# Kernel optimization log

Hardware: AMD Instinct MI355X
Metric: run time of the kernel (lower is better)

The kernel has to match this reference:

```python
import jax, jax.numpy as jnp
import numpy as np

# Geometry: 256x256 image, 16x16 superpixel grid (cell=16), K=256, C=20 features, B=4.
B, H, W, C, KG = 4, 256, 256, 20, 16
K = KG * KG
CELL = H // KG
BIG_DIST = 1e4  # additive distance for non-neighbor superpixels


def setup_inputs() -> dict:
    key = jax.random.key(0)
    kf, = jax.random.split(key, 1)
    # initial hard pixel->superpixel grid assignment (get_spixel_init)
    gy = jnp.arange(H) // CELL
    gx = jnp.arange(W) // CELL
    spixel_init = (gy[:, None] * KG + gx[None, :]).reshape(-1).astype(jnp.int32)  # [N]
    # 9-neighborhood validity mask (compute_neighbor_spix_idx)
    ky = jnp.arange(K) // KG
    kx = jnp.arange(K) % KG
    pgy = spixel_init // KG
    pgx = spixel_init % KG
    valid = ((jnp.abs(pgy[:, None] - ky[None, :]) <= 1)
             & (jnp.abs(pgx[:, None] - kx[None, :]) <= 1)).astype(jnp.float32)  # [N, K]
    adjust = (1.0 - valid) * BIG_DIST  # [N, K]
    features = jax.random.normal(kf, (B, H * W, C), dtype=jnp.float32)  # CNN output, flattened
    return {
        "features": features,
        "valid_spixel": valid,
        "adjust_dist": adjust,
        "spixel_init": spixel_init,
        "iter_EM": 10,
    }


def _e_step(mean, features, valid_spixel, adjust_dist):
    # squared distances via ||f||^2 - 2 f.m + ||m||^2 (bmm form)
    feat_sq = jnp.sum(features * features, axis=-1)        # [B, N]
    mean_sq = jnp.sum(mean * mean, axis=-1)                # [B, K]
    dot = jnp.einsum('bnc,bkc->bnk', features, mean)       # [B, N, K]
    dist_sq = feat_sq[:, :, None] - 2.0 * dot + mean_sq[:, None, :]
    dist_sq = dist_sq * valid_spixel[None] + adjust_dist[None]
    # std = 1/sqrt(2) => 2*std^2 = 1, so softmax argument is -dist_sq
    return jax.nn.softmax(-dist_sq, axis=2)                # [B, N, K]


def _m_step(features, posteriors):
    # L1-normalize posteriors over the pixel axis (dim=1), then weighted mean
    col = jnp.maximum(jnp.sum(posteriors, axis=1, keepdims=True), 1e-12)
    post_norm = posteriors / col
    return jnp.einsum('bnk,bnc->bkc', post_norm, features)  # [B, K, C]


def reference(features, valid_spixel, adjust_dist, spixel_init, iter_EM):
    # compute_init_spixel_feat: mean of features within each initial superpixel (detached in torch)
    n = features.shape[1]
    sums = jax.vmap(lambda f: jax.ops.segment_sum(f, spixel_init, num_segments=K))(features)  # [B, K, C]
    counts = jax.ops.segment_sum(jnp.ones((n,), features.dtype), spixel_init, num_segments=K)  # [K]
    mean = jax.lax.stop_gradient(sums / jnp.maximum(counts, 1.0)[None, :, None])
    for _ in range(int(iter_EM) - 1):
        posteriors = _e_step(mean, features, valid_spixel, adjust_dist)
        mean = _m_step(features, posteriors)
    return _e_step(mean, features, valid_spixel, adjust_dist)
```

## Files before the change

kernel.cpp:

```cpp
#include <hip/hip_runtime.h>
#include <hip/hip_cooperative_groups.h>


#define NBATCH 4
#define WIMG   256
#define NC     20
#define NCS    21
#define SCELL  32
#define NKG    16
#define NK     256
#define NPIX   65536
#define CELLSZ 16
#define LDST   260

__device__ __forceinline__ float dot4f(const float4 a, const float4 b) {
    return fmaf(a.x, b.x, fmaf(a.y, b.y, fmaf(a.z, b.z, a.w * b.w)));
}

__device__ __forceinline__ void load_feat(const float* __restrict__ feat, int b, int n, float f[NC]) {
    const float4* fp = (const float4*)(feat + ((size_t)b * NPIX + n) * NC);
    #pragma unroll
    for (int i = 0; i < 5; ++i) {
        float4 v = fp[i];
        f[4 * i + 0] = v.x; f[4 * i + 1] = v.y; f[4 * i + 2] = v.z; f[4 * i + 3] = v.w;
    }
}


__device__ __forceinline__ void gate(int* done, int target, int b, int cy, int cx, int t) {
    if (t < 25) {
        int dy = t / 5 - 2, dx = t % 5 - 2;
        int ky = cy + dy, kx = cx + dx;
        if (ky >= 0 && ky < NKG && kx >= 0 && kx < NKG) {
            int idx = b * NK + ky * NKG + kx;
            while (__hip_atomic_load(&done[idx], __ATOMIC_RELAXED, __HIP_MEMORY_SCOPE_AGENT) < target) {
                __builtin_amdgcn_s_sleep(1);
            }
        }
    }
    __syncthreads();
}

__device__ __forceinline__ void e_step_p(const float* f, int b, int cy, int cx,
                                         const float* __restrict__ Sprev,
                                         const float* rrL, const float* mtL, float p[9]) {
    float a[9];
    float amax = -1e30f;
    #pragma unroll
    for (int dy = -1; dy <= 1; ++dy) {
        #pragma unroll
        for (int dx = -1; dx <= 1; ++dx) {
            int j = (dy + 1) * 3 + (dx + 1);
            int ky = cy + dy, kx = cx + dx;
            if (ky >= 0 && ky < NKG && kx >= 0 && kx < NKG) {
                const float* sp = Sprev + ((size_t)(b * NK + ky * NKG + kx)) * SCELL;
                float dots = 0.f;
                #pragma unroll
                for (int c = 0; c < NC; ++c) dots = fmaf(f[c], sp[c], dots);
                a[j] = 2.0f * rrL[j] * dots - mtL[j];
                amax = fmaxf(amax, a[j]);
            } else {
                a[j] = -1e30f;
            }
        }
    }
    float esum = 0.f;
    #pragma unroll
    for (int j = 0; j < 9; ++j) {
        float e = (a[j] > -1e29f) ? __expf(a[j] - amax) : 0.0f;
        p[j] = e;
        esum += e;
    }
    float inv = 1.0f / esum;
    #pragma unroll
    for (int j = 0; j < 9; ++j) p[j] *= inv;
}

__global__ __launch_bounds__(256, 4) void k_ssn_df(const float* __restrict__ feat,
                                                   int* __restrict__ done,
                                                   float* __restrict__ Sbase,
                                                   float* __restrict__ out) {
    __shared__ float fT[NCS * LDST];
    __shared__ float pT[9 * LDST];
    __shared__ float part[21 * 8 * 9];
    __shared__ float rrL[9], mtL[9];

    const size_t SBUF = (size_t)NBATCH * NK * SCELL;
    int blk = blockIdx.x;
    int b = blk >> 8, k0 = blk & 255;
    int cy = k0 >> 4, cx = k0 & 15;
    int t = threadIdx.x;
    int ly = t >> 4, lx = t & 15;
    int n = (cy * CELLSZ + ly) * WIMG + cx * CELLSZ + lx;

    float f[NC];
    load_feat(feat, b, n, f);
    #pragma unroll
    for (int c = 0; c < NC; ++c) fT[c * LDST + t] = f[c];
    fT[NC * LDST + t] = 1.0f;
    __syncthreads();

    if (t < NCS) {
        float s;
        if (t == NC) {
            s = 256.0f;
        } else {
            s = 0.f;
            const float4* row = (const float4*)&fT[t * LDST];
            #pragma unroll 4
            for (int i = 0; i < 64; ++i) { float4 v = row[i]; s += v.x + v.y + v.z + v.w; }
        }
        __hip_atomic_store(&Sbase[((size_t)(b * NK + k0)) * SCELL + t], s,
                           __ATOMIC_RELAXED, __HIP_MEMORY_SCOPE_AGENT);
    }
    __syncthreads();
    if (t == 0) __hip_atomic_fetch_add(&done[blk], 1, __ATOMIC_RELAXED, __HIP_MEMORY_SCOPE_AGENT);

    for (int it = 1; it <= 9; ++it) {
        const float* __restrict__ Sprev = Sbase + (size_t)(it - 1) * SBUF;
        float* Snext = Sbase + (size_t)it * SBUF;

        gate(done, it, b, cy, cx, t);

        if (t < 9) {
            int dy = t / 3 - 1, dx = t % 3 - 1;
            int ky = cy + dy, kx = cx + dx;
            if (ky >= 0 && ky < NKG && kx >= 0 && kx < NKG) {
                const float* sp = Sprev + ((size_t)(b * NK + ky * NKG + kx)) * SCELL;
                float ssq = 0.f;
                #pragma unroll
                for (int c = 0; c < NC; ++c) ssq = fmaf(sp[c], sp[c], ssq);
                float r = 1.0f / fmaxf(sp[NC], 1e-12f);
                rrL[t] = r;
                mtL[t] = ssq * r * r;
            }
        }
        __syncthreads();

        float p[9];
        e_step_p(f, b, cy, cx, Sprev, rrL, mtL, p);
        #pragma unroll
        for (int j = 0; j < 9; ++j) pT[j * LDST + t] = p[j];
        __syncthreads();

        if (t < 168) {
            int tile = t >> 3, kid = t & 7;
            int j0 = (tile / 7) * 3, c0 = (tile % 7) * 3;
            float acc[3][3] = {};
            #pragma unroll
            for (int ch = 0; ch < 8; ++ch) {
                int nb = kid * 32 + (((ch + kid) & 7) << 2);
                float4 pv[3], fv[3];
                #pragma unroll
                for (int jj = 0; jj < 3; ++jj) pv[jj] = *(const float4*)&pT[(j0 + jj) * LDST + nb];
                #pragma unroll
                for (int cc = 0; cc < 3; ++cc) fv[cc] = *(const float4*)&fT[(c0 + cc) * LDST + nb];
                #pragma unroll
                for (int jj = 0; jj < 3; ++jj)
                    #pragma unroll
                    for (int cc = 0; cc < 3; ++cc)
                        acc[jj][cc] += dot4f(pv[jj], fv[cc]);
            }
            #pragma unroll
            for (int jj = 0; jj < 3; ++jj)
                #pragma unroll
                for (int cc = 0; cc < 3; ++cc)
                    part[tile * 72 + kid * 9 + jj * 3 + cc] = acc[jj][cc];
        }
        __syncthreads();
        if (t < 189) {
            int j = t / 21, c = t % 21;
            int tile = (j / 3) * 7 + (c / 3);
            int elem = (j % 3) * 3 + (c % 3);
            float s = 0.f;
            #pragma unroll
            for (int kid = 0; kid < 8; ++kid) s += part[tile * 72 + kid * 9 + elem];
            int ky = cy + (j / 3) - 1, kx = cx + (j % 3) - 1;
            if (ky >= 0 && ky < NKG && kx >= 0 && kx < NKG)
                atomicAdd(&Snext[((size_t)(b * NK + ky * NKG + kx)) * SCELL + c], s);
        }
        __syncthreads();
        if (t == 0) __hip_atomic_fetch_add(&done[blk], 1, __ATOMIC_RELAXED, __HIP_MEMORY_SCOPE_AGENT);
    }

    {
        const float* __restrict__ Sprev = Sbase + (size_t)9 * SBUF;
        gate(done, 10, b, cy, cx, t);
        if (t < 9) {
            int dy = t / 3 - 1, dx = t % 3 - 1;
            int ky = cy + dy, kx = cx + dx;
            if (ky >= 0 && ky < NKG && kx >= 0 && kx < NKG) {
                const float* sp = Sprev + ((size_t)(b * NK + ky * NKG + kx)) * SCELL;
                float ssq = 0.f;
                #pragma unroll
                for (int c = 0; c < NC; ++c) ssq = fmaf(sp[c], sp[c], ssq);
                float r = 1.0f / fmaxf(sp[NC], 1e-12f);
                rrL[t] = r;
                mtL[t] = ssq * r * r;
            }
        }
        __syncthreads();

        float p[9];
        e_step_p(f, b, cy, cx, Sprev, rrL, mtL, p);
        #pragma unroll
        for (int j = 0; j < 9; ++j) pT[j * LDST + t] = p[j];
        __syncthreads();

        int wv = t >> 6, ln = t & 63;
        int j4[4];
        #pragma unroll
        for (int q = 0; q < 4; ++q) {
            int k = 4 * ln + q;
            int ky = k >> 4, kx = k & 15;
            int dy = ky - cy, dx = kx - cx;
            j4[q] = (dy >= -1 && dy <= 1 && dx >= -1 && dx <= 1) ? (dy + 1) * 3 + (dx + 1) : -1;
        }
        for (int i = 0; i < 64; ++i) {
            int pix = wv * 64 + i;
            int py = pix >> 4, px = pix & 15;
            int np = (cy * CELLSZ + py) * WIMG + cx * CELLSZ + px;
            float4 o;
            o.x = (j4[0] >= 0) ? pT[j4[0] * LDST + pix] : 0.0f;
            o.y = (j4[1] >= 0) ? pT[j4[1] * LDST + pix] : 0.0f;
            o.z = (j4[2] >= 0) ? pT[j4[2] * LDST + pix] : 0.0f;
            o.w = (j4[3] >= 0) ? pT[j4[3] * LDST + pix] : 0.0f;
            size_t rowoff = ((size_t)(b * NPIX + np)) * (size_t)NK;
            *(float4*)(out + rowoff + 4 * ln) = o;
        }
    }
}

__device__ __forceinline__ void e_step_fb(const float* f, int b, int cy, int cx,
                                          const float* __restrict__ Sprev, float p[9]) {
    float a[9];
    float amax = -1e30f;
    #pragma unroll
    for (int dy = -1; dy <= 1; ++dy) {
        #pragma unroll
        for (int dx = -1; dx <= 1; ++dx) {
            int j = (dy + 1) * 3 + (dx + 1);
            int ky = cy + dy, kx = cx + dx;
            if (ky >= 0 && ky < NKG && kx >= 0 && kx < NKG) {
                const float* sp = Sprev + ((size_t)(b * NK + ky * NKG + kx)) * NCS;
                float dots = 0.f, ssq = 0.f;
                #pragma unroll
                for (int c = 0; c < NC; ++c) {
                    float sv = sp[c];
                    dots = fmaf(f[c], sv, dots);
                    ssq  = fmaf(sv, sv, ssq);
                }
                float col = fmaxf(sp[NC], 1e-12f);
                float r = 1.0f / col;
                a[j] = 2.0f * r * dots - (r * r) * ssq;
                amax = fmaxf(amax, a[j]);
            } else {
                a[j] = -1e30f;
            }
        }
    }
    float esum = 0.f;
    #pragma unroll
    for (int j = 0; j < 9; ++j) {
        float e = (a[j] > -1e29f) ? __expf(a[j] - amax) : 0.0f;
        p[j] = e;
        esum += e;
    }
    float inv = 1.0f / esum;
    #pragma unroll
    for (int j = 0; j < 9; ++j) p[j] *= inv;
}

__global__ __launch_bounds__(256, 4) void k_init(const float* __restrict__ feat,
                                                 float* __restrict__ S0,
                                                 float* __restrict__ S1) {
    __shared__ float fT[NC * LDST];
    int blk = blockIdx.x;
    int b = blk >> 8, k0 = blk & 255;
    int cy = k0 >> 4, cx = k0 & 15;
    int t = threadIdx.x;
    int ly = t >> 4, lx = t & 15;
    int n = (cy * CELLSZ + ly) * WIMG + cx * CELLSZ + lx;
    float f[NC];
    load_feat(feat, b, n, f);
    #pragma unroll
    for (int c = 0; c < NC; ++c) fT[c * LDST + t] = f[c];
    __syncthreads();
    if (t < NCS) {
        float s;
        if (t == NC) {
            s = 256.0f;
        } else {
            s = 0.f;
            const float4* row = (const float4*)&fT[t * LDST];
            #pragma unroll 4
            for (int i = 0; i < 64; ++i) { float4 v = row[i]; s += v.x + v.y + v.z + v.w; }
        }
        size_t off = ((size_t)(b * NK + k0)) * NCS + t;
        S0[off] = s;
        S1[off] = 0.0f;
    }
}

__global__ __launch_bounds__(256, 4) void k_em(const float* __restrict__ feat,
                                               const float* __restrict__ Sprev,
                                               float* __restrict__ Snext,
                                               float* __restrict__ Szero) {
    __shared__ float fT[NCS * LDST];
    __shared__ float pT[9 * LDST];
    __shared__ float part[21 * 8 * 9];
    int blk = blockIdx.x;
    int b = blk >> 8, k0 = blk & 255;
    int cy = k0 >> 4, cx = k0 & 15;
    int t = threadIdx.x;
    int ly = t >> 4, lx = t & 15;
    int n = (cy * CELLSZ + ly) * WIMG + cx * CELLSZ + lx;
    float f[NC];
    load_feat(feat, b, n, f);
    #pragma unroll
    for (int c = 0; c < NC; ++c) fT[c * LDST + t] = f[c];
    fT[NC * LDST + t] = 1.0f;
    float p[9];
    e_step_fb(f, b, cy, cx, Sprev, p);
    #pragma unroll
    for (int j = 0; j < 9; ++j) pT[j * LDST + t] = p[j];
    __syncthreads();
    if (t < 168) {
        int tile = t >> 3, kid = t & 7;
        int j0 = (tile / 7) * 3, c0 = (tile % 7) * 3;
        float acc[3][3] = {};
        #pragma unroll
        for (int ch = 0; ch < 8; ++ch) {
            int nb = kid * 32 + (((ch + kid) & 7) << 2);
            float4 pv[3], fv[3];
            #pragma unroll
            for (int jj = 0; jj < 3; ++jj) pv[jj] = *(const float4*)&pT[(j0 + jj) * LDST + nb];
            #pragma unroll
            for (int cc = 0; cc < 3; ++cc) fv[cc] = *(const float4*)&fT[(c0 + cc) * LDST + nb];
            #pragma unroll
            for (int jj = 0; jj < 3; ++jj)
                #pragma unroll
                for (int cc = 0; cc < 3; ++cc)
                    acc[jj][cc] += dot4f(pv[jj], fv[cc]);
        }
        #pragma unroll
        for (int jj = 0; jj < 3; ++jj)
            #pragma unroll
            for (int cc = 0; cc < 3; ++cc)
                part[tile * 72 + kid * 9 + jj * 3 + cc] = acc[jj][cc];
    }
    __syncthreads();
    if (t < 189) {
        int j = t / 21, c = t % 21;
        int tile = (j / 3) * 7 + (c / 3);
        int elem = (j % 3) * 3 + (c % 3);
        float s = 0.f;
        #pragma unroll
        for (int kid = 0; kid < 8; ++kid) s += part[tile * 72 + kid * 9 + elem];
        int ky = cy + (j / 3) - 1, kx = cx + (j % 3) - 1;
        if (ky >= 0 && ky < NKG && kx >= 0 && kx < NKG)
            atomicAdd(&Snext[((size_t)(b * NK + ky * NKG + kx)) * NCS + c], s);
    }
    if (t < NCS) Szero[((size_t)(b * NK + k0)) * NCS + t] = 0.0f;
}

__global__ __launch_bounds__(256, 4) void k_final(const float* __restrict__ feat,
                                                  const float* __restrict__ Sprev,
                                                  float* __restrict__ out) {
    __shared__ float pT[9 * LDST];
    int blk = blockIdx.x;
    int b = blk >> 8, k0 = blk & 255;
    int cy = k0 >> 4, cx = k0 & 15;
    int t = threadIdx.x;
    int ly = t >> 4, lx = t & 15;
    int n = (cy * CELLSZ + ly) * WIMG + cx * CELLSZ + lx;
    float f[NC];
    load_feat(feat, b, n, f);
    float p[9];
    e_step_fb(f, b, cy, cx, Sprev, p);
    #pragma unroll
    for (int j = 0; j < 9; ++j) pT[j * LDST + t] = p[j];
    __syncthreads();
    int wv = t >> 6, ln = t & 63;
    int j4[4];
    #pragma unroll
    for (int q = 0; q < 4; ++q) {
        int k = 4 * ln + q;
        int ky = k >> 4, kx = k & 15;
        int dy = ky - cy, dx = kx - cx;
        j4[q] = (dy >= -1 && dy <= 1 && dx >= -1 && dx <= 1) ? (dy + 1) * 3 + (dx + 1) : -1;
    }
    for (int i = 0; i < 64; ++i) {
        int pix = wv * 64 + i;
        int py = pix >> 4, px = pix & 15;
        int np = (cy * CELLSZ + py) * WIMG + cx * CELLSZ + px;
        float4 o;
        o.x = (j4[0] >= 0) ? pT[j4[0] * LDST + pix] : 0.0f;
        o.y = (j4[1] >= 0) ? pT[j4[1] * LDST + pix] : 0.0f;
        o.z = (j4[2] >= 0) ? pT[j4[2] * LDST + pix] : 0.0f;
        o.w = (j4[3] >= 0) ? pT[j4[3] * LDST + pix] : 0.0f;
        size_t rowoff = ((size_t)(b * NPIX + np)) * (size_t)NK;
        *(float4*)(out + rowoff + 4 * ln) = o;
    }
}

extern "C" void kernel_launch(void* const* d_in, const int* in_sizes, int n_in,
                              void* d_out, int out_size, void* d_ws, size_t ws_size,
                              hipStream_t stream) {
    (void)in_sizes; (void)n_in; (void)out_size;
    const float* feat = (const float*)d_in[0];
    float* out = (float*)d_out;

    int* done = (int*)d_ws;
    float* Sbase = (float*)((char*)d_ws + 4096);
    const size_t zbytes = 4096 + 10 * (size_t)NBATCH * NK * SCELL * sizeof(float);

    dim3 grid(NBATCH * NK), block(256);
    if (ws_size >= zbytes) {
        hipMemsetAsync(d_ws, 0, zbytes, stream);
        void* args[] = { (void*)&feat, (void*)&done, (void*)&Sbase, (void*)&out };
        hipError_t err = hipLaunchCooperativeKernel((const void*)k_ssn_df, grid, block, args, 0, stream);
        if (err == hipSuccess) return;
    }

    const size_t SB = (size_t)NBATCH * NK * NCS;
    float* s0 = (float*)d_ws;
    float* s1 = (float*)d_ws + SB;
    float* s2 = (float*)d_ws + 2 * SB;
    float* bufs[3] = { s0, s1, s2 };
    k_init<<<grid, block, 0, stream>>>(feat, bufs[0], bufs[1]);
    for (int i = 1; i <= 9; ++i)
        k_em<<<grid, block, 0, stream>>>(feat, bufs[(i - 1) % 3], bufs[i % 3], bufs[(i + 1) % 3]);
    k_final<<<grid, block, 0, stream>>>(feat, bufs[0], out);
}
```

Before: 673.7 us.

## Replace atomicAdd scatter with per-block partial stores and neighbor gather reduction

Each block now writes its 9x21 partial M-step sums to a private slot instead of doing float atomicAdds into neighbors' accumulators. A second neighbor-only gate lets each block gather its own superpixel sum from the 9 neighbors' partials. This removes atomic contention and the large workspace memset, since only the done counters are zeroed now. Other changes: the 3x3 superpixel stats are staged in shared memory, blocks are remapped to group rows per XCD, and the output uses nontemporal stores. The cost is twice as many gate waits per iteration.

```diff
diff --git a/kernel.cpp b/kernel.cpp
--- a/kernel.cpp
+++ b/kernel.cpp
@@ -6,15 +6,24 @@
 #define WIMG   256
 #define NC     20
 #define NCS    21
-#define SCELL  32
+#define PSTR   24
 #define NKG    16
 #define NK     256
 #define NPIX   65536
 #define CELLSZ 16
 #define LDST   260
 
+typedef float floatx4 __attribute__((ext_vector_type(4)));
+
 __device__ __forceinline__ float dot4f(const float4 a, const float4 b) {
     return fmaf(a.x, b.x, fmaf(a.y, b.y, fmaf(a.z, b.z, a.w * b.w)));
+}
+
+__device__ __forceinline__ float ld_sc1(const float* p) {
+    return __hip_atomic_load(p, __ATOMIC_RELAXED, __HIP_MEMORY_SCOPE_AGENT);
+}
+__device__ __forceinline__ void st_sc1(float* p, float v) {
+    __hip_atomic_store(p, v, __ATOMIC_RELAXED, __HIP_MEMORY_SCOPE_AGENT);
 }
 
 __device__ __forceinline__ void load_feat(const float* __restrict__ feat, int b, int n, float f[NC]) {
@@ -26,24 +35,22 @@
     }
 }
 
-
-__device__ __forceinline__ void gate(int* done, int target, int b, int cy, int cx, int t) {
-    if (t < 25) {
-        int dy = t / 5 - 2, dx = t % 5 - 2;
-        int ky = cy + dy, kx = cx + dx;
+__device__ __forceinline__ void gate9(int* done, int target, int b, int cy, int cx, int t) {
+    if (t < 9) {
+        int ky = cy + t / 3 - 1, kx = cx + t % 3 - 1;
         if (ky >= 0 && ky < NKG && kx >= 0 && kx < NKG) {
             int idx = b * NK + ky * NKG + kx;
             while (__hip_atomic_load(&done[idx], __ATOMIC_RELAXED, __HIP_MEMORY_SCOPE_AGENT) < target) {
-                __builtin_amdgcn_s_sleep(1);
+                __builtin_amdgcn_s_sleep(2);
             }
         }
     }
     __syncthreads();
 }
 
-__device__ __forceinline__ void e_step_p(const float* f, int b, int cy, int cx,
-                                         const float* __restrict__ Sprev,
-                                         const float* rrL, const float* mtL, float p[9]) {
+__device__ __forceinline__ void e_step_l(const float* f, int cy, int cx,
+                                         const float* sS, const float* rrL, const float* mtL,
+                                         float p[9]) {
     float a[9];
     float amax = -1e30f;
     #pragma unroll
@@ -53,7 +60,7 @@
             int j = (dy + 1) * 3 + (dx + 1);
             int ky = cy + dy, kx = cx + dx;
             if (ky >= 0 && ky < NKG && kx >= 0 && kx < NKG) {
-                const float* sp = Sprev + ((size_t)(b * NK + ky * NKG + kx)) * SCELL;
+                const float* sp = sS + j * PSTR;
                 float dots = 0.f;
                 #pragma unroll
                 for (int c = 0; c < NC; ++c) dots = fmaf(f[c], sp[c], dots);
@@ -76,19 +83,22 @@
     for (int j = 0; j < 9; ++j) p[j] *= inv;
 }
 
-__global__ __launch_bounds__(256, 4) void k_ssn_df(const float* __restrict__ feat,
-                                                   int* __restrict__ done,
-                                                   float* __restrict__ Sbase,
-                                                   float* __restrict__ out) {
+__global__ __launch_bounds__(256, 4) void k_ssn_g(const float* __restrict__ feat,
+                                                  int* __restrict__ done,
+                                                  float* __restrict__ Sc,
+                                                  float* __restrict__ Pp,
+                                                  float* __restrict__ out) {
     __shared__ float fT[NCS * LDST];
     __shared__ float pT[9 * LDST];
     __shared__ float part[21 * 8 * 9];
+    __shared__ float sS[9 * PSTR];
     __shared__ float rrL[9], mtL[9];
 
-    const size_t SBUF = (size_t)NBATCH * NK * SCELL;
     int blk = blockIdx.x;
-    int b = blk >> 8, k0 = blk & 255;
-    int cy = k0 >> 4, cx = k0 & 15;
+    int xcd = blk & 7, q = blk >> 3;
+    int b = q >> 5, r = q & 31;
+    int cy = (xcd << 1) | (r >> 4), cx = r & 15;
+    int k0 = cy * NKG + cx;
     int t = threadIdx.x;
     int ly = t >> 4, lx = t & 15;
     int n = (cy * CELLSZ + ly) * WIMG + cx * CELLSZ + lx;
@@ -110,35 +120,41 @@
             #pragma unroll 4
             for (int i = 0; i < 64; ++i) { float4 v = row[i]; s += v.x + v.y + v.z + v.w; }
         }
-        __hip_atomic_store(&Sbase[((size_t)(b * NK + k0)) * SCELL + t], s,
-                           __ATOMIC_RELAXED, __HIP_MEMORY_SCOPE_AGENT);
-    }
-    __syncthreads();
-    if (t == 0) __hip_atomic_fetch_add(&done[blk], 1, __ATOMIC_RELAXED, __HIP_MEMORY_SCOPE_AGENT);
+        st_sc1(&Sc[((size_t)(b * NK + k0)) * PSTR + t], s);
+    }
+    __syncthreads();
+    if (t == 0) __hip_atomic_fetch_add(&done[b * NK + k0], 1, __ATOMIC_RELAXED, __HIP_MEMORY_SCOPE_AGENT);
 
     for (int it = 1; it <= 9; ++it) {
-        const float* __restrict__ Sprev = Sbase + (size_t)(it - 1) * SBUF;
-        float* Snext = Sbase + (size_t)it * SBUF;
-
-        gate(done, it, b, cy, cx, t);
-
+        const float* Sp = Sc + ((size_t)(it - 1) * NBATCH + b) * NK * PSTR;
+        float* Pit = Pp + ((size_t)it * NBATCH + b) * NK * 9 * PSTR;
+        float* Snx = Sc + ((size_t)it * NBATCH + b) * NK * PSTR;
+
+        gate9(done, 2 * it - 1, b, cy, cx, t);
+
+        if (t < 189) {
+            int j = t / 21, c = t % 21;
+            int ky = cy + j / 3 - 1, kx = cx + j % 3 - 1;
+            if (ky >= 0 && ky < NKG && kx >= 0 && kx < NKG)
+                sS[j * PSTR + c] = ld_sc1(&Sp[(size_t)(ky * NKG + kx) * PSTR + c]);
+        }
+        __syncthreads();
         if (t < 9) {
-            int dy = t / 3 - 1, dx = t % 3 - 1;
-            int ky = cy + dy, kx = cx + dx;
+            int ky = cy + t / 3 - 1, kx = cx + t % 3 - 1;
             if (ky >= 0 && ky < NKG && kx >= 0 && kx < NKG) {
-                const float* sp = Sprev + ((size_t)(b * NK + ky * NKG + kx)) * SCELL;
+                const float* sp = &sS[t * PSTR];
                 float ssq = 0.f;
                 #pragma unroll
                 for (int c = 0; c < NC; ++c) ssq = fmaf(sp[c], sp[c], ssq);
-                float r = 1.0f / fmaxf(sp[NC], 1e-12f);
-                rrL[t] = r;
-                mtL[t] = ssq * r * r;
-            }
+                float rr = 1.0f / fmaxf(sp[NC], 1e-12f);
+                rrL[t] = rr;
+                mtL[t] = ssq * rr * rr;
+            } else { rrL[t] = 1.0f; mtL[t] = 0.0f; }
         }
         __syncthreads();
 
         float p[9];
-        e_step_p(f, b, cy, cx, Sprev, rrL, mtL, p);
+        e_step_l(f, cy, cx, sS, rrL, mtL, p);
         #pragma unroll
         for (int j = 0; j < 9; ++j) pT[j * LDST + t] = p[j];
         __syncthreads();
@@ -175,34 +191,60 @@
             float s = 0.f;
             #pragma unroll
             for (int kid = 0; kid < 8; ++kid) s += part[tile * 72 + kid * 9 + elem];
-            int ky = cy + (j / 3) - 1, kx = cx + (j % 3) - 1;
+            int ky = cy + j / 3 - 1, kx = cx + j % 3 - 1;
             if (ky >= 0 && ky < NKG && kx >= 0 && kx < NKG)
-                atomicAdd(&Snext[((size_t)(b * NK + ky * NKG + kx)) * SCELL + c], s);
-        }
-        __syncthreads();
-        if (t == 0) __hip_atomic_fetch_add(&done[blk], 1, __ATOMIC_RELAXED, __HIP_MEMORY_SCOPE_AGENT);
+                st_sc1(&Pit[((size_t)k0 * 9 + j) * PSTR + c], s);
+        }
+        __syncthreads();
+        if (t == 0) __hip_atomic_fetch_add(&done[b * NK + k0], 1, __ATOMIC_RELAXED, __HIP_MEMORY_SCOPE_AGENT);
+
+        gate9(done, 2 * it, b, cy, cx, t);
+
+        if (t < NCS) {
+            float s = 0.f;
+            #pragma unroll
+            for (int u = -1; u <= 1; ++u) {
+                #pragma unroll
+                for (int v = -1; v <= 1; ++v) {
+                    int py = cy + u, px = cx + v;
+                    if (py >= 0 && py < NKG && px >= 0 && px < NKG) {
+                        int e = (1 - u) * 3 + (1 - v);
+                        s += ld_sc1(&Pit[((size_t)(py * NKG + px) * 9 + e) * PSTR + t]);
+                    }
+                }
+            }
+            st_sc1(&Snx[(size_t)k0 * PSTR + t], s);
+        }
+        __syncthreads();
+        if (t == 0) __hip_atomic_fetch_add(&done[b * NK + k0], 1, __ATOMIC_RELAXED, __HIP_MEMORY_SCOPE_AGENT);
     }
 
     {
-        const float* __restrict__ Sprev = Sbase + (size_t)9 * SBUF;
-        gate(done, 10, b, cy, cx, t);
+        const float* Sp = Sc + ((size_t)9 * NBATCH + b) * NK * PSTR;
+        gate9(done, 19, b, cy, cx, t);
+        if (t < 189) {
+            int j = t / 21, c = t % 21;
+            int ky = cy + j / 3 - 1, kx = cx + j % 3 - 1;
+            if (ky >= 0 && ky < NKG && kx >= 0 && kx < NKG)
+                sS[j * PSTR + c] = ld_sc1(&Sp[(size_t)(ky * NKG + kx) * PSTR + c]);
+        }
+        __syncthreads();
         if (t < 9) {
-            int dy = t / 3 - 1, dx = t % 3 - 1;
-            int ky = cy + dy, kx = cx + dx;
+            int ky = cy + t / 3 - 1, kx = cx + t % 3 - 1;
             if (ky >= 0 && ky < NKG && kx >= 0 && kx < NKG) {
-                const float* sp = Sprev + ((size_t)(b * NK + ky * NKG + kx)) * SCELL;
+                const float* sp = &sS[t * PSTR];
                 float ssq = 0.f;
                 #pragma unroll
                 for (int c = 0; c < NC; ++c) ssq = fmaf(sp[c], sp[c], ssq);
-                float r = 1.0f / fmaxf(sp[NC], 1e-12f);
-                rrL[t] = r;
-                mtL[t] = ssq * r * r;
-            }
+                float rr = 1.0f / fmaxf(sp[NC], 1e-12f);
+                rrL[t] = rr;
+                mtL[t] = ssq * rr * rr;
+            } else { rrL[t] = 1.0f; mtL[t] = 0.0f; }
         }
         __syncthreads();
 
         float p[9];
-        e_step_p(f, b, cy, cx, Sprev, rrL, mtL, p);
+        e_step_l(f, cy, cx, sS, rrL, mtL, p);
         #pragma unroll
         for (int j = 0; j < 9; ++j) pT[j * LDST + t] = p[j];
         __syncthreads();
@@ -210,23 +252,23 @@
         int wv = t >> 6, ln = t & 63;
         int j4[4];
         #pragma unroll
-        for (int q = 0; q < 4; ++q) {
-            int k = 4 * ln + q;
+        for (int q2 = 0; q2 < 4; ++q2) {
+            int k = 4 * ln + q2;
             int ky = k >> 4, kx = k & 15;
             int dy = ky - cy, dx = kx - cx;
-            j4[q] = (dy >= -1 && dy <= 1 && dx >= -1 && dx <= 1) ? (dy + 1) * 3 + (dx + 1) : -1;
+            j4[q2] = (dy >= -1 && dy <= 1 && dx >= -1 && dx <= 1) ? (dy + 1) * 3 + (dx + 1) : -1;
         }
         for (int i = 0; i < 64; ++i) {
             int pix = wv * 64 + i;
             int py = pix >> 4, px = pix & 15;
             int np = (cy * CELLSZ + py) * WIMG + cx * CELLSZ + px;
-            float4 o;
+            floatx4 o;
             o.x = (j4[0] >= 0) ? pT[j4[0] * LDST + pix] : 0.0f;
             o.y = (j4[1] >= 0) ? pT[j4[1] * LDST + pix] : 0.0f;
             o.z = (j4[2] >= 0) ? pT[j4[2] * LDST + pix] : 0.0f;
             o.w = (j4[3] >= 0) ? pT[j4[3] * LDST + pix] : 0.0f;
             size_t rowoff = ((size_t)(b * NPIX + np)) * (size_t)NK;
-            *(float4*)(out + rowoff + 4 * ln) = o;
+            __builtin_nontemporal_store(o, (floatx4*)(out + rowoff + 4 * ln));
         }
     }
 }
@@ -251,8 +293,8 @@
                     ssq  = fmaf(sv, sv, ssq);
                 }
                 float col = fmaxf(sp[NC], 1e-12f);
-                float r = 1.0f / col;
-                a[j] = 2.0f * r * dots - (r * r) * ssq;
+                float rr = 1.0f / col;
+                a[j] = 2.0f * rr * dots - (rr * rr) * ssq;
                 amax = fmaxf(amax, a[j]);
             } else {
                 a[j] = -1e30f;
@@ -412,14 +454,17 @@
     float* out = (float*)d_out;
 
     int* done = (int*)d_ws;
-    float* Sbase = (float*)((char*)d_ws + 4096);
-    const size_t zbytes = 4096 + 10 * (size_t)NBATCH * NK * SCELL * sizeof(float);
+    float* Sc = (float*)((char*)d_ws + 4096);
+    const size_t SC_FLOATS = (size_t)10 * NBATCH * NK * PSTR;
+    float* Pp = Sc + SC_FLOATS;
+    const size_t PP_FLOATS = (size_t)10 * NBATCH * NK * 9 * PSTR;
+    const size_t zneed = 4096 + (SC_FLOATS + PP_FLOATS) * sizeof(float);
 
     dim3 grid(NBATCH * NK), block(256);
-    if (ws_size >= zbytes) {
-        hipMemsetAsync(d_ws, 0, zbytes, stream);
-        void* args[] = { (void*)&feat, (void*)&done, (void*)&Sbase, (void*)&out };
-        hipError_t err = hipLaunchCooperativeKernel((const void*)k_ssn_df, grid, block, args, 0, stream);
+    if (ws_size >= zneed) {
+        (void)hipMemsetAsync(d_ws, 0, 4096, stream);
+        void* args[] = { (void*)&feat, (void*)&done, (void*)&Sc, (void*)&Pp, (void*)&out };
+        hipError_t err = hipLaunchCooperativeKernel((const void*)k_ssn_g, grid, block, args, 0, stream);
         if (err == hipSuccess) return;
     }
 
```

After: 775.7 us. +15.1%, slower.
